# Kernel optimization log

Hardware: AMD Instinct MI355X
Metric: run time of the kernel (lower is better)

The kernel has to match this reference:

```python
import jax, jax.numpy as jnp
import numpy as np

B, T, D, H, E = 16, 4096, 256, 512, 8


def setup_inputs() -> dict:
    key = jax.random.key(0)
    ks = jax.random.split(key, 5)
    x = jax.random.normal(ks[0], (B, T, D), dtype=jnp.float32)
    gate_w = jax.random.normal(ks[1], (D, E), dtype=jnp.float32) * 0.02
    gate_b = jnp.zeros((E,), dtype=jnp.float32)
    W1 = jax.random.normal(ks[2], (E, D, H), dtype=jnp.float32) * 0.02
    b1 = jnp.zeros((E, H), dtype=jnp.float32)
    W2 = jax.random.normal(ks[3], (E, H, D), dtype=jnp.float32) * 0.02
    b2 = jnp.zeros((E, D), dtype=jnp.float32)
    return {"x": x, "gate_w": gate_w, "gate_b": gate_b,
            "W1": W1, "b1": b1, "W2": W2, "b2": b2}


def reference(x, gate_w, gate_b, W1, b1, W2, b2):
    Bb, Tt, Dd = x.shape
    Ee = gate_w.shape[1]
    xf = x.reshape(-1, Dd)                       # [N, D]
    N = xf.shape[0]
    logits = xf @ gate_w + gate_b                # [N, E]
    probs = jax.nn.softmax(logits, axis=-1)
    top2_vals, top2_idx = jax.lax.top_k(probs, 2)  # [N, 2]
    # combine weights: w[n, e] = sum_k top2_vals[n,k] * (top2_idx[n,k]==e)
    cw = jnp.zeros((N, Ee), dtype=xf.dtype).at[
        jnp.arange(N)[:, None], top2_idx].add(top2_vals)  # [N, E]

    def step(acc, params):
        w1, bb1, w2, bb2, we = params            # per-expert slices
        h = jax.nn.gelu(xf @ w1 + bb1, approximate=False)  # [N, H]
        y = h @ w2 + bb2                          # [N, D]
        return acc + we[:, None] * y, None

    out, _ = jax.lax.scan(step, jnp.zeros_like(xf),
                          (W1, b1, W2, b2, cw.T))
    return out.reshape(Bb, Tt, Dd)
```

## Files before the change

### kernel.cpp

```cpp
#include <hip/hip_runtime.h>
#include <hip/hip_bf16.h>
#include <math.h>


#define N_TOK 65536
#define D_DIM 256
#define H_DIM 512
#define TILE_R 32
#define GRID_TILES 2112

typedef __bf16 bf16x8 __attribute__((ext_vector_type(8)));
typedef float f32x4 __attribute__((ext_vector_type(4)));

static __device__ __forceinline__ ushort f2bf(float f) {
    __hip_bfloat16 h = __float2bfloat16(f);
    ushort u;
    __builtin_memcpy(&u, &h, 2);
    return u;
}

static __device__ __forceinline__ float gelu(float v) {
    const float a = fabsf(v) * 0.70710678118654752f;
    const float t = __builtin_amdgcn_rcpf(fmaf(a, 0.47047f, 1.0f));
    const float p = t * fmaf(t, fmaf(t, 0.7478556f, -0.0958798f), 0.3480242f);
    const float er = fmaf(-p, __expf(-a * a), 1.0f);
    const float s = copysignf(er, v);
    return 0.5f * v * (1.0f + s);
}

__global__ __launch_bounds__(256) void prep(const float* __restrict__ x,
                                            const float* __restrict__ gate_w,
                                            const float* __restrict__ gate_b,
                                            const float* __restrict__ W1,
                                            const float* __restrict__ W2,
                                            ushort* __restrict__ xb,
                                            ushort* __restrict__ W1p,
                                            ushort* __restrict__ W2p,
                                            int* __restrict__ counts,
                                            int* __restrict__ pid_arr,
                                            float2* __restrict__ pw_arr) {
    __shared__ float gws[2048];
    __shared__ int lc[64];

    const int bid = blockIdx.x;
    const int tid = threadIdx.x;

    if (bid >= 2048) {
        const int pid = bid - 2048;
        const int t = (pid & 511) * 256 + tid;
        const int l = t & 63;
        const int lo = l & 15, hi = l >> 4;
        ushort v[8];
        if (pid < 512) {
            const int kb = (t >> 6) & 7;
            const int nb = (t >> 9) & 31;
            const int e  = t >> 14;
            const int k0 = kb * 32 + hi * 8;
            const int n  = nb * 16 + lo;
            const float* src = W1 + (size_t)e * D_DIM * H_DIM + n;
            #pragma unroll
            for (int j = 0; j < 8; ++j)
                v[j] = f2bf(src[(size_t)(k0 + j) * H_DIM]);
            *(uint4*)(W1p + (size_t)t * 8) = *(const uint4*)v;
        } else {
            const int kb = (t >> 6) & 15;
            const int nb = (t >> 10) & 15;
            const int e  = t >> 14;
            const int k0 = kb * 32 + hi * 8;
            const int n  = nb * 16 + lo;
            const float* src = W2 + (size_t)e * H_DIM * D_DIM + n;
            #pragma unroll
            for (int j = 0; j < 8; ++j)
                v[j] = f2bf(src[(size_t)(k0 + j) * D_DIM]);
            *(uint4*)(W2p + (size_t)t * 8) = *(const uint4*)v;
        }
        return;
    }

    const size_t t0 = (size_t)bid * 32;
    for (int i = tid; i < 2048; i += 256) gws[i] = gate_w[i];
    if (tid < 64) lc[tid] = 0;
    __syncthreads();

    const int m = tid >> 3, q = tid & 7;
    const float4* xr = (const float4*)(x + (t0 + m) * D_DIM + q * 32);
    ushort4* xw = (ushort4*)(xb + (t0 + m) * D_DIM + q * 32);

    double lg[8] = {0, 0, 0, 0, 0, 0, 0, 0};
    #pragma unroll
    for (int it = 0; it < 8; ++it) {
        const float4 v = xr[it];
        ushort4 bv;
        bv.x = f2bf(v.x); bv.y = f2bf(v.y); bv.z = f2bf(v.z); bv.w = f2bf(v.w);
        xw[it] = bv;
        const float* g = &gws[(q * 32 + it * 4) * 8];
        const float vv[4] = {v.x, v.y, v.z, v.w};
        #pragma unroll
        for (int j = 0; j < 4; ++j) {
            const double xv = (double)vv[j];
            #pragma unroll
            for (int e2 = 0; e2 < 8; ++e2) lg[e2] += xv * (double)g[j * 8 + e2];
        }
    }
    #pragma unroll
    for (int e2 = 0; e2 < 8; ++e2) {
        lg[e2] += __shfl_xor(lg[e2], 1, 64);
        lg[e2] += __shfl_xor(lg[e2], 2, 64);
        lg[e2] += __shfl_xor(lg[e2], 4, 64);
    }

    if (q == 0) {
        int e0 = 0, e1 = -1;
        #pragma unroll
        for (int e2 = 0; e2 < 8; ++e2) lg[e2] += (double)gate_b[e2];
        double b0 = -1e300, b1v = -1e300;
        #pragma unroll
        for (int e2 = 0; e2 < 8; ++e2)
            if (lg[e2] > b0) { b0 = lg[e2]; e0 = e2; }
        #pragma unroll
        for (int e2 = 0; e2 < 8; ++e2)
            if (e2 != e0 && lg[e2] > b1v) { b1v = lg[e2]; e1 = e2; }
        double s = 0;
        #pragma unroll
        for (int e2 = 0; e2 < 8; ++e2) s += exp(lg[e2] - b0);
        const float p0 = (float)(1.0 / s);
        const float p1 = (float)(exp(b1v - b0) / s);
        const int pid = e0 * 8 + e1;
        atomicAdd(&lc[pid], 1);
        const int tok = (int)t0 + m;
        pid_arr[tok] = pid;
        pw_arr[tok] = make_float2(p0, p1);
    }
    __syncthreads();
    if (tid < 64 && lc[tid]) atomicAdd(&counts[tid], lc[tid]);
}

__global__ __launch_bounds__(256) void scatter(const int* __restrict__ counts,
                                               const int* __restrict__ pid_arr,
                                               const float2* __restrict__ pw_arr,
                                               int* __restrict__ cursor,
                                               int* __restrict__ tok_list,
                                               float* __restrict__ w0l,
                                               float* __restrict__ w1l) {
    __shared__ int lcnt[64];
    __shared__ int lbase[64];
    const int tid = threadIdx.x;
    const int t = blockIdx.x * 256 + tid;
    if (tid < 64) lcnt[tid] = 0;
    __syncthreads();
    const int pid = pid_arr[t];
    const float2 pw = pw_arr[t];
    const int lpos = atomicAdd(&lcnt[pid], 1);
    __syncthreads();
    if (tid < 64) {
        int s = 0;
        for (int i = 0; i < tid; ++i) s += counts[i];
        const int mine = lcnt[tid];
        lbase[tid] = s + (mine ? atomicAdd(&cursor[tid], mine) : 0);
    }
    __syncthreads();
    const int pos = lbase[pid] + lpos;
    tok_list[pos] = t;
    w0l[pos] = pw.x;
    w1l[pos] = pw.y;
}

__global__ __launch_bounds__(512, 4) void moe_expert(const ushort* __restrict__ xb,
                                                     const ushort* __restrict__ W1p,
                                                     const ushort* __restrict__ W2p,
                                                     const float* __restrict__ b1,
                                                     const float* __restrict__ b2,
                                                     const int* __restrict__ counts,
                                                     const int* __restrict__ tok_list,
                                                     const float* __restrict__ w0l,
                                                     const float* __restrict__ w1l,
                                                     float* __restrict__ out) {
    __shared__ __align__(16) char Xs[TILE_R * 512];
    __shared__ __align__(16) char Hs[TILE_R * 1024];
    __shared__ int   toks[TILE_R];
    __shared__ float wgt[2][TILE_R];

    int n = 0;
    for (int i = 0; i < 64; ++i) n += (counts[i] + 31) >> 5;
    const int qn = n >> 3, rn = n & 7;
    const int xc = blockIdx.x & 7, ix = blockIdx.x >> 3;
    if (ix >= qn + (xc < rn ? 1 : 0)) return;
    const int wg = xc * qn + min(xc, rn) + ix;

    int pid = -1, row0 = 0, nv = 0, gbase = 0;
    int st = 0, sc = 0;
    for (int i = 0; i < 64; ++i) {
        const int c = counts[i];
        const int nt = (c + 31) >> 5;
        if (pid < 0 && wg < st + nt) { pid = i; row0 = (wg - st) << 5; nv = min(TILE_R, c - row0); gbase = sc; }
        st += nt; sc += c;
    }
    const int ea = pid >> 3, eb = pid & 7;
    const int gidx = gbase + row0;

    const int tid = threadIdx.x;
    const int w = tid >> 6, l = tid & 63;
    const int lo = l & 15, hi = l >> 4;

    if (tid < TILE_R) {
        const bool vld = tid < nv;
        const int src = gidx + (vld ? tid : 0);
        toks[tid]   = tok_list[src];
        wgt[0][tid] = vld ? w0l[src] : 0.f;
        wgt[1][tid] = vld ? w1l[src] : 0.f;
    }

    {
        const int r = tid >> 4;
        const int tk = tok_list[gidx + min(r, nv - 1)];
        const char* src = (const char*)(xb + (size_t)tk * D_DIM) + (tid & 15) * 32;
        const int bo = (tid & 15) * 32, sw = (r & 7) << 4;
        const uint4 a0 = *(const uint4*)src;
        const uint4 a1 = *(const uint4*)(src + 16);
        *(uint4*)(Xs + r * 512 + (bo ^ sw)) = a0;
        *(uint4*)(Xs + r * 512 + ((bo + 16) ^ sw)) = a1;
    }
    __syncthreads();

    f32x4 acc2[2][2];
    #pragma unroll
    for (int mi = 0; mi < 2; ++mi)
        #pragma unroll
        for (int ni = 0; ni < 2; ++ni)
            acc2[mi][ni] = (f32x4){0.f, 0.f, 0.f, 0.f};

    #pragma unroll
    for (int ph = 0; ph < 2; ++ph) {
        const int ew = ph ? eb : ea;

        #pragma unroll
        for (int pass = 0; pass < 2; ++pass) {
            const int nb0 = w * 4 + pass * 2;
            const char* w1b = (const char*)W1p + (size_t)(ew * 32 + nb0) * 8192 + (size_t)l * 16;

            f32x4 acc1[2][2];
            #pragma unroll
            for (int nb = 0; nb < 2; ++nb)
                #pragma unroll
                for (int tb = 0; tb < 2; ++tb)
                    acc1[nb][tb] = (f32x4){0.f, 0.f, 0.f, 0.f};

            bf16x8 wf[3][2];
            #pragma unroll
            for (int nb = 0; nb < 2; ++nb) {
                wf[0][nb] = *(const bf16x8*)(w1b + nb * 8192);
                wf[1][nb] = *(const bf16x8*)(w1b + nb * 8192 + 1024);
            }

            #pragma unroll
            for (int ks = 0; ks < 8; ++ks) {
                const int cb = ks % 3;
                if (ks < 6) {
                    const int lb = (ks + 2) % 3;
                    wf[lb][0] = *(const bf16x8*)(w1b + (ks + 2) * 1024);
                    wf[lb][1] = *(const bf16x8*)(w1b + 8192 + (ks + 2) * 1024);
                }
                #pragma unroll
                for (int tb = 0; tb < 2; ++tb) {
                    const int slot = tb * 16 + lo;
                    const bf16x8 xf = *(const bf16x8*)(Xs + slot * 512 +
                                      ((ks * 64 + hi * 16) ^ ((slot & 7) << 4)));
                    __builtin_amdgcn_s_setprio(1);
                    #pragma unroll
                    for (int nb = 0; nb < 2; ++nb)
                        acc1[nb][tb] = __builtin_amdgcn_mfma_f32_16x16x32_bf16(wf[cb][nb], xf, acc1[nb][tb], 0, 0, 0);
                    __builtin_amdgcn_s_setprio(0);
                }
            }

            #pragma unroll
            for (int nb = 0; nb < 2; ++nb) {
                const int hc = (nb0 + nb) * 16 + hi * 4;
                const float4 b1q = *(const float4*)(b1 + ew * H_DIM + hc);
                #pragma unroll
                for (int tb = 0; tb < 2; ++tb) {
                    const int slot = tb * 16 + lo;
                    const float wt = wgt[ph][slot];
                    ushort4 hv;
                    hv.x = f2bf(gelu(acc1[nb][tb][0] + b1q.x) * wt);
                    hv.y = f2bf(gelu(acc1[nb][tb][1] + b1q.y) * wt);
                    hv.z = f2bf(gelu(acc1[nb][tb][2] + b1q.z) * wt);
                    hv.w = f2bf(gelu(acc1[nb][tb][3] + b1q.w) * wt);
                    *(ushort4*)(Hs + slot * 1024 + ((hc * 2) ^ ((slot & 7) << 4))) = hv;
                }
            }
        }
        __syncthreads();

        const char* w2b = (const char*)W2p + (size_t)(ew * 16 + w * 2) * 16384 + (size_t)l * 16;
        bf16x8 wf2[3][2];
        #pragma unroll
        for (int ni = 0; ni < 2; ++ni) {
            wf2[0][ni] = *(const bf16x8*)(w2b + ni * 16384);
            wf2[1][ni] = *(const bf16x8*)(w2b + ni * 16384 + 1024);
        }

        #pragma unroll
        for (int ks = 0; ks < 16; ++ks) {
            const int cb = ks % 3;
            if (ks < 14) {
                const int lb = (ks + 2) % 3;
                wf2[lb][0] = *(const bf16x8*)(w2b + (ks + 2) * 1024);
                wf2[lb][1] = *(const bf16x8*)(w2b + 16384 + (ks + 2) * 1024);
            }
            #pragma unroll
            for (int mi = 0; mi < 2; ++mi) {
                const int slot = mi * 16 + lo;
                const bf16x8 hf = *(const bf16x8*)(Hs + slot * 1024 +
                                  ((ks * 64 + hi * 16) ^ ((slot & 7) << 4)));
                __builtin_amdgcn_s_setprio(1);
                #pragma unroll
                for (int ni = 0; ni < 2; ++ni)
                    acc2[mi][ni] = __builtin_amdgcn_mfma_f32_16x16x32_bf16(hf, wf2[cb][ni], acc2[mi][ni], 0, 0, 0);
                __builtin_amdgcn_s_setprio(0);
            }
        }
        if (ph == 0) __syncthreads();
    }

    #pragma unroll
    for (int ni = 0; ni < 2; ++ni) {
        const int col = w * 32 + ni * 16 + lo;
        const float b2a = b2[ea * D_DIM + col];
        const float b2b = b2[eb * D_DIM + col];
        #pragma unroll
        for (int mi = 0; mi < 2; ++mi) {
            #pragma unroll
            for (int rg = 0; rg < 4; ++rg) {
                const int r = mi * 16 + hi * 4 + rg;
                if (r < nv) {
                    const float v = acc2[mi][ni][rg] + wgt[0][r] * b2a + wgt[1][r] * b2b;
                    out[(size_t)toks[r] * D_DIM + col] = v;
                }
            }
        }
    }
}

extern "C" void kernel_launch(void* const* d_in, const int* in_sizes, int n_in,
                              void* d_out, int out_size, void* d_ws, size_t ws_size,
                              hipStream_t stream) {
    const float* x      = (const float*)d_in[0];
    const float* gate_w = (const float*)d_in[1];
    const float* gate_b = (const float*)d_in[2];
    const float* W1     = (const float*)d_in[3];
    const float* b1     = (const float*)d_in[4];
    const float* W2     = (const float*)d_in[5];
    const float* b2     = (const float*)d_in[6];
    float* out = (float*)d_out;

    char* ws = (char*)d_ws;
    ushort* xb      = (ushort*)(ws);
    ushort* W1p     = (ushort*)(ws + 33554432);
    ushort* W2p     = (ushort*)(ws + 35651584);
    int*    pid_arr = (int*)   (ws + 37748736);
    float2* pw_arr  = (float2*)(ws + 38010880);
    int*    tok_lst = (int*)   (ws + 38535168);
    float*  w0l     = (float*) (ws + 38797312);
    float*  w1l     = (float*) (ws + 39059456);
    int*    counts  = (int*)   (ws + 39321600);
    int*    cursor  = (int*)   (ws + 39321856);

    hipMemsetAsync(counts, 0, 512, stream);

    prep<<<dim3(3072), 256, 0, stream>>>(x, gate_w, gate_b, W1, W2,
                                         xb, W1p, W2p, counts, pid_arr, pw_arr);
    scatter<<<dim3(256), 256, 0, stream>>>(counts, pid_arr, pw_arr, cursor,
                                           tok_lst, w0l, w1l);
    moe_expert<<<dim3(GRID_TILES), 512, 0, stream>>>(xb, W1p, W2p, b1, b2, counts,
                                                     tok_lst, w0l, w1l, out);
}
```

Measured before the change: 204.1 us.

## Double token tile to 64 rows and chunk hidden dimension in halves

The token tile per workgroup grows from 32 to 64 rows, so each weight fragment loaded from global memory feeds twice as many MFMA ops. To keep LDS size unchanged, the hidden dimension is processed in two 256-wide chunks per expert, with the GELU intermediate stored in a half-size buffer and the second GEMM accumulating across chunks. The cost is more barriers per tile, more accumulator registers, larger padding waste on partially filled 64-row tiles, and fewer workgroups to spread across CUs. The W2 prefetch is also deepened to a 4-slot ring.

```diff
diff --git a/kernel.cpp b/kernel.cpp
--- a/kernel.cpp
+++ b/kernel.cpp
@@ -6,8 +6,8 @@
 #define N_TOK 65536
 #define D_DIM 256
 #define H_DIM 512
-#define TILE_R 32
-#define GRID_TILES 2112
+#define TILE_R 64
+#define GRID_TILES 1088
 
 typedef __bf16 bf16x8 __attribute__((ext_vector_type(8)));
 typedef float f32x4 __attribute__((ext_vector_type(4)));
@@ -176,12 +176,12 @@
                                                      const float* __restrict__ w1l,
                                                      float* __restrict__ out) {
     __shared__ __align__(16) char Xs[TILE_R * 512];
-    __shared__ __align__(16) char Hs[TILE_R * 1024];
+    __shared__ __align__(16) char Hs[TILE_R * 512];
     __shared__ int   toks[TILE_R];
     __shared__ float wgt[2][TILE_R];
 
     int n = 0;
-    for (int i = 0; i < 64; ++i) n += (counts[i] + 31) >> 5;
+    for (int i = 0; i < 64; ++i) n += (counts[i] + 63) >> 6;
     const int qn = n >> 3, rn = n & 7;
     const int xc = blockIdx.x & 7, ix = blockIdx.x >> 3;
     if (ix >= qn + (xc < rn ? 1 : 0)) return;
@@ -191,8 +191,8 @@
     int st = 0, sc = 0;
     for (int i = 0; i < 64; ++i) {
         const int c = counts[i];
-        const int nt = (c + 31) >> 5;
-        if (pid < 0 && wg < st + nt) { pid = i; row0 = (wg - st) << 5; nv = min(TILE_R, c - row0); gbase = sc; }
+        const int nt = (c + 63) >> 6;
+        if (pid < 0 && wg < st + nt) { pid = i; row0 = (wg - st) << 6; nv = min(TILE_R, c - row0); gbase = sc; }
         st += nt; sc += c;
     }
     const int ea = pid >> 3, eb = pid & 7;
@@ -211,107 +211,106 @@
     }
 
     {
-        const int r = tid >> 4;
+        const int r = tid >> 3;
         const int tk = tok_list[gidx + min(r, nv - 1)];
-        const char* src = (const char*)(xb + (size_t)tk * D_DIM) + (tid & 15) * 32;
-        const int bo = (tid & 15) * 32, sw = (r & 7) << 4;
-        const uint4 a0 = *(const uint4*)src;
-        const uint4 a1 = *(const uint4*)(src + 16);
-        *(uint4*)(Xs + r * 512 + (bo ^ sw)) = a0;
-        *(uint4*)(Xs + r * 512 + ((bo + 16) ^ sw)) = a1;
-    }
-    __syncthreads();
-
-    f32x4 acc2[2][2];
-    #pragma unroll
-    for (int mi = 0; mi < 2; ++mi)
+        const char* src = (const char*)(xb + (size_t)tk * D_DIM) + (tid & 7) * 64;
+        char* dst = Xs + r * 512;
+        const int bo = (tid & 7) * 64, sw = (r & 7) << 4;
+        #pragma unroll
+        for (int c = 0; c < 4; ++c)
+            *(uint4*)(dst + ((bo + c * 16) ^ sw)) = *(const uint4*)(src + c * 16);
+    }
+    __syncthreads();
+
+    f32x4 acc2[4][2];
+    #pragma unroll
+    for (int mi = 0; mi < 4; ++mi)
         #pragma unroll
         for (int ni = 0; ni < 2; ++ni)
             acc2[mi][ni] = (f32x4){0.f, 0.f, 0.f, 0.f};
 
     #pragma unroll
-    for (int ph = 0; ph < 2; ++ph) {
+    for (int phase = 0; phase < 4; ++phase) {
+        const int ph = phase >> 1, ch = phase & 1;
         const int ew = ph ? eb : ea;
 
-        #pragma unroll
-        for (int pass = 0; pass < 2; ++pass) {
-            const int nb0 = w * 4 + pass * 2;
-            const char* w1b = (const char*)W1p + (size_t)(ew * 32 + nb0) * 8192 + (size_t)l * 16;
-
-            f32x4 acc1[2][2];
-            #pragma unroll
-            for (int nb = 0; nb < 2; ++nb)
+        const char* w1b = (const char*)W1p + (size_t)(ew * 32 + ch * 16 + w * 2) * 8192 + (size_t)l * 16;
+
+        f32x4 acc1[2][4];
+        #pragma unroll
+        for (int nb = 0; nb < 2; ++nb)
+            #pragma unroll
+            for (int tb = 0; tb < 4; ++tb)
+                acc1[nb][tb] = (f32x4){0.f, 0.f, 0.f, 0.f};
+
+        bf16x8 wf[3][2];
+        #pragma unroll
+        for (int nb = 0; nb < 2; ++nb) {
+            wf[0][nb] = *(const bf16x8*)(w1b + nb * 8192);
+            wf[1][nb] = *(const bf16x8*)(w1b + nb * 8192 + 1024);
+        }
+
+        #pragma unroll
+        for (int ks = 0; ks < 8; ++ks) {
+            const int cb = ks % 3;
+            if (ks < 6) {
+                const int lb = (ks + 2) % 3;
+                wf[lb][0] = *(const bf16x8*)(w1b + (ks + 2) * 1024);
+                wf[lb][1] = *(const bf16x8*)(w1b + 8192 + (ks + 2) * 1024);
+            }
+            #pragma unroll
+            for (int tb = 0; tb < 4; ++tb) {
+                const int slot = tb * 16 + lo;
+                const bf16x8 xf = *(const bf16x8*)(Xs + slot * 512 +
+                                  ((ks * 64 + hi * 16) ^ ((slot & 7) << 4)));
+                __builtin_amdgcn_s_setprio(1);
                 #pragma unroll
-                for (int tb = 0; tb < 2; ++tb)
-                    acc1[nb][tb] = (f32x4){0.f, 0.f, 0.f, 0.f};
-
-            bf16x8 wf[3][2];
-            #pragma unroll
-            for (int nb = 0; nb < 2; ++nb) {
-                wf[0][nb] = *(const bf16x8*)(w1b + nb * 8192);
-                wf[1][nb] = *(const bf16x8*)(w1b + nb * 8192 + 1024);
-            }
-
-            #pragma unroll
-            for (int ks = 0; ks < 8; ++ks) {
-                const int cb = ks % 3;
-                if (ks < 6) {
-                    const int lb = (ks + 2) % 3;
-                    wf[lb][0] = *(const bf16x8*)(w1b + (ks + 2) * 1024);
-                    wf[lb][1] = *(const bf16x8*)(w1b + 8192 + (ks + 2) * 1024);
-                }
-                #pragma unroll
-                for (int tb = 0; tb < 2; ++tb) {
-                    const int slot = tb * 16 + lo;
-                    const bf16x8 xf = *(const bf16x8*)(Xs + slot * 512 +
-                                      ((ks * 64 + hi * 16) ^ ((slot & 7) << 4)));
-                    __builtin_amdgcn_s_setprio(1);
-                    #pragma unroll
-                    for (int nb = 0; nb < 2; ++nb)
-                        acc1[nb][tb] = __builtin_amdgcn_mfma_f32_16x16x32_bf16(wf[cb][nb], xf, acc1[nb][tb], 0, 0, 0);
-                    __builtin_amdgcn_s_setprio(0);
-                }
-            }
-
-            #pragma unroll
-            for (int nb = 0; nb < 2; ++nb) {
-                const int hc = (nb0 + nb) * 16 + hi * 4;
-                const float4 b1q = *(const float4*)(b1 + ew * H_DIM + hc);
-                #pragma unroll
-                for (int tb = 0; tb < 2; ++tb) {
-                    const int slot = tb * 16 + lo;
-                    const float wt = wgt[ph][slot];
-                    ushort4 hv;
-                    hv.x = f2bf(gelu(acc1[nb][tb][0] + b1q.x) * wt);
-                    hv.y = f2bf(gelu(acc1[nb][tb][1] + b1q.y) * wt);
-                    hv.z = f2bf(gelu(acc1[nb][tb][2] + b1q.z) * wt);
-                    hv.w = f2bf(gelu(acc1[nb][tb][3] + b1q.w) * wt);
-                    *(ushort4*)(Hs + slot * 1024 + ((hc * 2) ^ ((slot & 7) << 4))) = hv;
-                }
+                for (int nb = 0; nb < 2; ++nb)
+                    acc1[nb][tb] = __builtin_amdgcn_mfma_f32_16x16x32_bf16(wf[cb][nb], xf, acc1[nb][tb], 0, 0, 0);
+                __builtin_amdgcn_s_setprio(0);
+            }
+        }
+
+        #pragma unroll
+        for (int nb = 0; nb < 2; ++nb) {
+            const int hcE = (ch * 16 + w * 2 + nb) * 16 + hi * 4;
+            const int hcH = (w * 2 + nb) * 16 + hi * 4;
+            const float4 b1q = *(const float4*)(b1 + ew * H_DIM + hcE);
+            #pragma unroll
+            for (int tb = 0; tb < 4; ++tb) {
+                const int slot = tb * 16 + lo;
+                const float wt = wgt[ph][slot];
+                ushort4 hv;
+                hv.x = f2bf(gelu(acc1[nb][tb][0] + b1q.x) * wt);
+                hv.y = f2bf(gelu(acc1[nb][tb][1] + b1q.y) * wt);
+                hv.z = f2bf(gelu(acc1[nb][tb][2] + b1q.z) * wt);
+                hv.w = f2bf(gelu(acc1[nb][tb][3] + b1q.w) * wt);
+                *(ushort4*)(Hs + slot * 512 + ((hcH * 2) ^ ((slot & 7) << 4))) = hv;
             }
         }
         __syncthreads();
 
-        const char* w2b = (const char*)W2p + (size_t)(ew * 16 + w * 2) * 16384 + (size_t)l * 16;
-        bf16x8 wf2[3][2];
-        #pragma unroll
-        for (int ni = 0; ni < 2; ++ni) {
-            wf2[0][ni] = *(const bf16x8*)(w2b + ni * 16384);
-            wf2[1][ni] = *(const bf16x8*)(w2b + ni * 16384 + 1024);
-        }
-
-        #pragma unroll
-        for (int ks = 0; ks < 16; ++ks) {
-            const int cb = ks % 3;
-            if (ks < 14) {
-                const int lb = (ks + 2) % 3;
-                wf2[lb][0] = *(const bf16x8*)(w2b + (ks + 2) * 1024);
-                wf2[lb][1] = *(const bf16x8*)(w2b + 16384 + (ks + 2) * 1024);
-            }
-            #pragma unroll
-            for (int mi = 0; mi < 2; ++mi) {
+        const char* w2b = (const char*)W2p + ((size_t)(ew * 16 + w * 2) * 16 + ch * 8) * 1024 + (size_t)l * 16;
+
+        bf16x8 wf2[4][2];
+        #pragma unroll
+        for (int p = 0; p < 3; ++p) {
+            wf2[p][0] = *(const bf16x8*)(w2b + p * 1024);
+            wf2[p][1] = *(const bf16x8*)(w2b + 16384 + p * 1024);
+        }
+
+        #pragma unroll
+        for (int ks = 0; ks < 8; ++ks) {
+            const int cb = ks & 3;
+            if (ks < 5) {
+                const int lb = (ks + 3) & 3;
+                wf2[lb][0] = *(const bf16x8*)(w2b + (ks + 3) * 1024);
+                wf2[lb][1] = *(const bf16x8*)(w2b + 16384 + (ks + 3) * 1024);
+            }
+            #pragma unroll
+            for (int mi = 0; mi < 4; ++mi) {
                 const int slot = mi * 16 + lo;
-                const bf16x8 hf = *(const bf16x8*)(Hs + slot * 1024 +
+                const bf16x8 hf = *(const bf16x8*)(Hs + slot * 512 +
                                   ((ks * 64 + hi * 16) ^ ((slot & 7) << 4)));
                 __builtin_amdgcn_s_setprio(1);
                 #pragma unroll
@@ -320,7 +319,7 @@
                 __builtin_amdgcn_s_setprio(0);
             }
         }
-        if (ph == 0) __syncthreads();
+        if (phase < 3) __syncthreads();
     }
 
     #pragma unroll
@@ -329,7 +328,7 @@
         const float b2a = b2[ea * D_DIM + col];
         const float b2b = b2[eb * D_DIM + col];
         #pragma unroll
-        for (int mi = 0; mi < 2; ++mi) {
+        for (int mi = 0; mi < 4; ++mi) {
             #pragma unroll
             for (int rg = 0; rg < 4; ++rg) {
                 const int r = mi * 16 + hi * 4 + rg;
```

Result: slower. 212.7 us (+4.3%).
